# Kernel tuning notes

Hardware: AMD Instinct MI355X
Metric: run time of the kernel (lower is better)

## Reference

```python
import jax, jax.numpy as jnp
import numpy as np

L, H, C, V, BLK = 6, 16, 1024, 32000, 2048
B, T, TA = 2, 512, 512
DFF = 4 * C
STD = 0.02
PROJ_STD = 0.02 / np.sqrt(2 * L)  # c_proj init per module
SCALE = 1.0 / np.sqrt(C // H)


def setup_inputs() -> dict:
    key = jax.random.key(0)
    ks = iter(jax.random.split(key, 64))
    nrm = lambda shape, std=STD: jax.random.normal(next(ks), shape, jnp.float32) * std
    inp = {
        'idx': jax.random.randint(next(ks), (B, T), 0, V),
        'xa': jax.random.normal(next(ks), (B, TA, C), jnp.float32),
        'wte': nrm((V, C)),            # tied with lm_head
        'wpe': nrm((BLK, C)),
        'ln1_w': jnp.ones((L, C)), 'ln1_b': jnp.zeros((L, C)),
        'sa_wq': nrm((L, C, C)), 'sa_bq': jnp.zeros((L, C)),
        'sa_wk': nrm((L, C, C)), 'sa_bk': jnp.zeros((L, C)),
        'sa_wv': nrm((L, C, C)), 'sa_bv': jnp.zeros((L, C)),
        'sa_wo': nrm((L, C, C), PROJ_STD), 'sa_bo': jnp.zeros((L, C)),
        'ca_wq': nrm((L, C, C)), 'ca_bq': jnp.zeros((L, C)),
        'ca_wk': nrm((L, C, C)), 'ca_bk': jnp.zeros((L, C)),
        'ca_wv': nrm((L, C, C)), 'ca_bv': jnp.zeros((L, C)),
        'ca_wo': nrm((L, C, C), PROJ_STD), 'ca_bo': jnp.zeros((L, C)),
        'ln2_w': jnp.ones((L, C)), 'ln2_b': jnp.zeros((L, C)),
        'fc_w': nrm((L, C, DFF)), 'fc_b': jnp.zeros((L, DFF)),
        'pr_w': nrm((L, DFF, C), PROJ_STD), 'pr_b': jnp.zeros((L, C)),
        'lnf_w': jnp.ones((C,)), 'lnf_b': jnp.zeros((C,)),
    }
    return inp


def _ln(h, w, b):
    m = h.mean(-1, keepdims=True)
    v = jnp.mean((h - m) ** 2, -1, keepdims=True)
    return (h - m) * jax.lax.rsqrt(v + 1e-5) * w + b


def _gelu(h):  # new_gelu (tanh approximation)
    return 0.5 * h * (1.0 + jnp.tanh(np.sqrt(2.0 / np.pi) * (h + 0.044715 * h ** 3)))


def _attn(hq, hkv, wq, bq, wk, bk, wv, bv, wo, bo):
    # NB: the original applies a tril causal mask even for cross-attention.
    Bq, Tq, _ = hq.shape
    Tk = hkv.shape[1]
    D = C // H
    q = (hq @ wq + bq).reshape(Bq, Tq, H, D)
    k = (hkv @ wk + bk).reshape(Bq, Tk, H, D)
    v = (hkv @ wv + bv).reshape(Bq, Tk, H, D)
    att = jnp.einsum('bqhd,bkhd->bhqk', q, k) * SCALE
    mask = jnp.tril(jnp.ones((Tq, Tk), bool))
    att = jnp.where(mask, att, -jnp.inf)
    att = jax.nn.softmax(att, axis=-1)
    y = jnp.einsum('bhqk,bkhd->bqhd', att, v).reshape(Bq, Tq, C)
    return y @ wo + bo


def _forward(idx, xa, wte, wpe, ln1_w, ln1_b, sa_wq, sa_bq, sa_wk, sa_bk, sa_wv, sa_bv, sa_wo, sa_bo,
             ca_wq, ca_bq, ca_wk, ca_bk, ca_wv, ca_bv, ca_wo, ca_bo,
             ln2_w, ln2_b, fc_w, fc_b, pr_w, pr_b, lnf_w, lnf_b):
    t = idx.shape[1]
    x = wte[idx] + wpe[:t][None]  # [B,T,C]

    def block(h, p):
        (l1w, l1b, sqw, sqb, skw, skb, svw, svb, sow, sob,
         cqw, cqb, ckw, ckb, cvw, cvb, cow, cob,
         l2w, l2b, fw, fb, pw, pb) = p
        n = _ln(h, l1w, l1b)
        h = h + _attn(n, n, sqw, sqb, skw, skb, svw, svb, sow, sob)
        n = _ln(h, l1w, l1b)  # ln_1 reused for cross-attn, as in source
        h = h + _attn(n, xa, cqw, cqb, ckw, ckb, cvw, cvb, cow, cob)
        n = _ln(h, l2w, l2b)
        h = h + (_gelu(n @ fw + fb) @ pw + pb)
        return h, None

    xs = (ln1_w, ln1_b, sa_wq, sa_bq, sa_wk, sa_bk, sa_wv, sa_bv, sa_wo, sa_bo,
          ca_wq, ca_bq, ca_wk, ca_bk, ca_wv, ca_bv, ca_wo, ca_bo,
          ln2_w, ln2_b, fc_w, fc_b, pr_w, pr_b)
    x, _ = jax.lax.scan(block, x, xs)
    x = _ln(x, lnf_w, lnf_b)
    return x @ wte.T  # tied lm_head, [B,T,V]


def reference(idx, xa, wte, wpe, ln1_w, ln1_b, sa_wq, sa_bq, sa_wk, sa_bk, sa_wv, sa_bv, sa_wo, sa_bo,
              ca_wq, ca_bq, ca_wk, ca_bk, ca_wv, ca_bv, ca_wo, ca_bo,
              ln2_w, ln2_b, fc_w, fc_b, pr_w, pr_b, lnf_w, lnf_b):
    return _forward(idx, xa, wte, wpe, ln1_w, ln1_b, sa_wq, sa_bq, sa_wk, sa_bk, sa_wv, sa_bv, sa_wo, sa_bo,
                    ca_wq, ca_bq, ca_wk, ca_bk, ca_wv, ca_bv, ca_wo, ca_bo,
                    ln2_w, ln2_b, fc_w, fc_b, pr_w, pr_b, lnf_w, lnf_b)
```

## Files before the change

### kernel.cpp

```cpp
#include <hip/hip_runtime.h>
#include <math.h>

#define CC   1024
#define HH   16
#define DH   64
#define TT   512
#define NTOK 1024
#define DFF_ 4096
#define VV   32000
#define QKSCALE 0.125f

typedef unsigned short u16;
typedef __attribute__((ext_vector_type(8))) short short8;
typedef __attribute__((ext_vector_type(4))) float f32x4;

__device__ __forceinline__ u16 f2bf(float f) {
  union { float f; unsigned u; } v; v.f = f;
  unsigned r = v.u + 0x7FFFu + ((v.u >> 16) & 1u);
  return (u16)(r >> 16);
}
__device__ __forceinline__ float gelu_f(float h) {
  return 0.5f * h * (1.0f + tanhf(0.7978845608028654f * (h + 0.044715f * h * h * h)));
}

template <int N> __device__ __forceinline__ void waitcnt_vm() {
  if constexpr (N == 0) asm volatile("s_waitcnt vmcnt(0)" ::: "memory");
  else if constexpr (N == 1) asm volatile("s_waitcnt vmcnt(1)" ::: "memory");
  else if constexpr (N == 2) asm volatile("s_waitcnt vmcnt(2)" ::: "memory");
  else if constexpr (N == 3) asm volatile("s_waitcnt vmcnt(3)" ::: "memory");
  else if constexpr (N == 4) asm volatile("s_waitcnt vmcnt(4)" ::: "memory");
  else if constexpr (N == 5) asm volatile("s_waitcnt vmcnt(5)" ::: "memory");
  else if constexpr (N == 6) asm volatile("s_waitcnt vmcnt(6)" ::: "memory");
  else if constexpr (N == 7) asm volatile("s_waitcnt vmcnt(7)" ::: "memory");
  else if constexpr (N == 8) asm volatile("s_waitcnt vmcnt(8)" ::: "memory");
  else static_assert(N <= 8, "unsupported vmcnt");
}

#define GLD16(gp, lp) __builtin_amdgcn_global_load_lds( \
    (const __attribute__((address_space(1))) void*)(gp), \
    (__attribute__((address_space(3))) void*)(lp), 16, 0, 0)

#define MFMA(a, b, c) __builtin_amdgcn_mfma_f32_16x16x32_bf16(a, b, c, 0, 0, 0)

__global__ __launch_bounds__(256) void embed_kernel(
    const int* __restrict__ idx, const float* __restrict__ wte,
    const float* __restrict__ wpe, float* __restrict__ x) {
  int row = blockIdx.x;
  int t = row & (TT - 1);
  int id = idx[row];
  const float4* a = (const float4*)(wte + (size_t)id * CC);
  const float4* p = (const float4*)(wpe + (size_t)t * CC);
  float4* o = (float4*)(x + (size_t)row * CC);
  int c = threadIdx.x;
  float4 va = a[c], vp = p[c];
  float4 ov;
  ov.x = va.x + vp.x; ov.y = va.y + vp.y; ov.z = va.z + vp.z; ov.w = va.w + vp.w;
  o[c] = ov;
}

__global__ __launch_bounds__(256) void ln_kernel(
    const float* __restrict__ x, const float* __restrict__ w,
    const float* __restrict__ b, u16* __restrict__ out) {
  int row = blockIdx.x, tid = threadIdx.x;
  float4 v = ((const float4*)(x + (size_t)row * CC))[tid];
  float s  = v.x + v.y + v.z + v.w;
  float sq = fmaf(v.x, v.x, fmaf(v.y, v.y, fmaf(v.z, v.z, v.w * v.w)));
  for (int o = 32; o > 0; o >>= 1) { s += __shfl_down(s, o); sq += __shfl_down(sq, o); }
  __shared__ float rs[4], rq[4];
  int wid = tid >> 6, lane = tid & 63;
  if (lane == 0) { rs[wid] = s; rq[wid] = sq; }
  __syncthreads();
  s  = rs[0] + rs[1] + rs[2] + rs[3];
  sq = rq[0] + rq[1] + rq[2] + rq[3];
  float mean = s * (1.0f / CC);
  float var  = sq * (1.0f / CC) - mean * mean;
  float rstd = 1.0f / sqrtf(var + 1e-5f);
  float4 wv = ((const float4*)w)[tid];
  float4 bv = ((const float4*)b)[tid];
  ushort4 o;
  o.x = f2bf((v.x - mean) * rstd * wv.x + bv.x);
  o.y = f2bf((v.y - mean) * rstd * wv.y + bv.y);
  o.z = f2bf((v.z - mean) * rstd * wv.z + bv.z);
  o.w = f2bf((v.w - mean) * rstd * wv.w + bv.w);
  ((ushort4*)(out + (size_t)row * CC))[tid] = o;
}

__global__ __launch_bounds__(256) void wtransL_kernel(
    const float* __restrict__ w0, const float* __restrict__ w1,
    const float* __restrict__ w2, const float* __restrict__ w3,
    const float* __restrict__ w4, const float* __restrict__ w5,
    const float* __restrict__ w6, const float* __restrict__ w7,
    const float* __restrict__ fc, const float* __restrict__ pr,
    u16* __restrict__ wt, size_t dls, int lbase) {
  const size_t M1 = 1048576;
  int z = blockIdx.z;
  int l = lbase + (z >> 4), slot = z & 15;
  size_t wofs = (size_t)l * M1;
  size_t mofs = (size_t)l * 4 * M1;
  const float* src;
  size_t doff = (size_t)(l - lbase) * dls;
  int sstr, dstr;
  if (slot < 8) {
    const float* base = slot == 0 ? w0 : slot == 1 ? w1 : slot == 2 ? w2
                      : slot == 3 ? w3 : slot == 4 ? w4 : slot == 5 ? w5
                      : slot == 6 ? w6 : w7;
    src = base + wofs; sstr = 1024; doff += (size_t)slot * M1; dstr = 1024;
  } else if (slot < 12) {
    int s = slot - 8;
    src = fc + mofs + (size_t)s * 1024; sstr = 4096;
    doff += 8 * M1 + (size_t)s * M1; dstr = 1024;
  } else {
    int s = slot - 12;
    src = pr + mofs + (size_t)s * M1; sstr = 1024;
    doff += 12 * M1 + (size_t)s * 1024; dstr = 4096;
  }
  __shared__ float t[64][65];
  int bx = blockIdx.x * 64, by = blockIdx.y * 64;
  int tid = threadIdx.x;
  int r16 = tid >> 4;
  int c4  = (tid & 15) * 4;
#pragma unroll
  for (int i = 0; i < 4; ++i) {
    int row = r16 + i * 16;
    float4 v = *(const float4*)&src[(size_t)(by + row) * sstr + bx + c4];
    t[row][c4] = v.x; t[row][c4 + 1] = v.y; t[row][c4 + 2] = v.z; t[row][c4 + 3] = v.w;
  }
  __syncthreads();
#pragma unroll
  for (int i = 0; i < 4; ++i) {
    int orow = r16 + i * 16;
    ushort4 o;
    o.x = f2bf(t[c4 + 0][orow]);
    o.y = f2bf(t[c4 + 1][orow]);
    o.z = f2bf(t[c4 + 2][orow]);
    o.w = f2bf(t[c4 + 3][orow]);
    *(ushort4*)&wt[doff + (size_t)(bx + orow) * dstr + by + c4] = o;
  }
}

__global__ __launch_bounds__(256) void convbf_kernel(
    const float* __restrict__ in, u16* __restrict__ out, int n4) {
  int i = blockIdx.x * 256 + threadIdx.x;
  if (i < n4) {
    float4 v = ((const float4*)in)[i];
    ushort4 o; o.x = f2bf(v.x); o.y = f2bf(v.y); o.z = f2bf(v.z); o.w = f2bf(v.w);
    ((ushort4*)out)[i] = o;
  }
}

template <int EPI, int MODE, int BM, int BN, int BK, int SK>
__global__ __launch_bounds__(256) void gemm_bf16_kernel(
    const u16* __restrict__ A, const u16* __restrict__ A2,
    const u16* __restrict__ B, const u16* __restrict__ B2,
    const float* __restrict__ bias, const float* __restrict__ bias2,
    const float* __restrict__ bias3, float* __restrict__ Cm,
    int K, int ldc, int whichbase) {
  constexpr int WM = BM / 2, WN = BN / 2, MF = WM / 16, NF = WN / 16;
  constexpr int KS = BK / 32;
  constexpr int NB = BK / 8;
  constexpr int PA = BM * BK / 2048;
  constexpr int PB = BN * BK / 2048;
  constexpr int RPP = 2048 / BK;
  constexpr int NBUF = (MODE == 2) ? 2 : (MODE == 4 ? 1 : 3);
  __shared__ u16 As[NBUF][BM * BK];
  __shared__ u16 Bs[NBUF][BN * BK];
  int tid = threadIdx.x;
  int lane = tid & 63, wave = tid >> 6;
  int wr = wave >> 1, wc = wave & 1;
  int row0, col0;
  bool isq = true;
  const u16* Ause = A;
  const u16* Buse = B;
  if (MODE == 2 || MODE == 4) {
    int id = blockIdx.x;
    int wg = (id & 7) * 250 + (id >> 3);
    row0 = (wg & 7) * BM;
    col0 = (wg >> 3) * BN;
  } else if (MODE == 3) {
    int bx = blockIdx.x;
    isq = bx < (1024 / BN);
    Ause = isq ? A : A2;
    Buse = isq ? B : B2;
    col0 = (isq ? bx : bx - 1024 / BN) * BN;
    row0 = blockIdx.y * BM;
  } else {
    row0 = blockIdx.y * BM;
    col0 = blockIdx.x * BN;
  }
  const int split = (SK > 1) ? blockIdx.z : 0;
  const int Kloc = K / SK;
  const int kbase = split * Kloc;
  f32x4 acc[MF][NF];
#pragma unroll
  for (int m = 0; m < MF; ++m)
#pragma unroll
    for (int n = 0; n < NF; ++n) acc[m][n] = (f32x4){0.f, 0.f, 0.f, 0.f};

  int srow = tid / NB;
  int sblk = (BK == 64) ? ((tid & 7) ^ ((tid >> 3) & 7))
                        : ((tid & 3) ^ ((tid >> 3) & 3));
  const u16* Ab = Ause + (size_t)row0 * K + kbase;
  int arow = wr * WM + (lane & 15);
  int brow = wc * WN + (lane & 15);
  int g8 = lane >> 4;
  const int NT = Kloc / BK;

  auto compute = [&](const u16* Ac, const u16* Bc) {
#pragma unroll
    for (int ks = 0; ks < KS; ++ks) {
      short8 af[MF], bg[NF];
#pragma unroll
      for (int m = 0; m < MF; ++m) {
        int row = arow + m * 16;
        int off = (BK == 64) ? row * 64 + (((ks * 4 + g8) ^ (row & 7)) << 3)
                             : row * 32 + ((g8 ^ ((row >> 1) & 3)) << 3);
        af[m] = *(const short8*)&Ac[off];
      }
#pragma unroll
      for (int n = 0; n < NF; ++n) {
        int row = brow + n * 16;
        int off = (BK == 64) ? row * 64 + (((ks * 4 + g8) ^ (row & 7)) << 3)
                             : row * 32 + ((g8 ^ ((row >> 1) & 3)) << 3);
        bg[n] = *(const short8*)&Bc[off];
      }
      __builtin_amdgcn_s_setprio(1);
#pragma unroll
      for (int m = 0; m < MF; ++m)
#pragma unroll
        for (int n = 0; n < NF; ++n)
          acc[m][n] = MFMA(af[m], bg[n], acc[m][n]);
      __builtin_amdgcn_s_setprio(0);
    }
  };

  if constexpr (MODE == 2) {
    const float* Bf = (const float*)B;
    int bsr = tid >> 2;
    int bkb = tid & 3;
    float4 rb0, rb1, rb2, rb3;
    auto loadB = [&](int k0) {
      const float* p0 = Bf + (size_t)(col0 + bsr) * 1024 + k0 + bkb * 8;
      const float* p1 = Bf + (size_t)(col0 + 64 + bsr) * 1024 + k0 + bkb * 8;
      rb0 = *(const float4*)p0; rb1 = *(const float4*)(p0 + 4);
      rb2 = *(const float4*)p1; rb3 = *(const float4*)(p1 + 4);
    };
    auto writeB = [&](int bufi) {
      u16 t0[8] = {f2bf(rb0.x), f2bf(rb0.y), f2bf(rb0.z), f2bf(rb0.w),
                   f2bf(rb1.x), f2bf(rb1.y), f2bf(rb1.z), f2bf(rb1.w)};
      u16 t1[8] = {f2bf(rb2.x), f2bf(rb2.y), f2bf(rb2.z), f2bf(rb2.w),
                   f2bf(rb3.x), f2bf(rb3.y), f2bf(rb3.z), f2bf(rb3.w)};
      int r1 = 64 + bsr;
      *(short8*)&Bs[bufi][bsr * 32 + ((bkb ^ ((bsr >> 1) & 3)) << 3)] = *(short8*)t0;
      *(short8*)&Bs[bufi][r1 * 32 + ((bkb ^ ((r1 >> 1) & 3)) << 3)] = *(short8*)t1;
    };
    auto stageA = [&](int bufi, int k0) {
#pragma unroll
      for (int p = 0; p < PA; ++p)
        GLD16(Ab + (size_t)(p * RPP + srow) * K + k0 + sblk * 8,
              &As[bufi][p * 2048 + wave * 512]);
    };
    loadB(0);
    stageA(0, 0);
    writeB(0);
    __syncthreads();
    for (int t = 0; t < NT; ++t) {
      int cur = t & 1;
      if (t + 1 < NT) { loadB((t + 1) * BK); stageA(cur ^ 1, (t + 1) * BK); }
      compute(As[cur], Bs[cur]);
      if (t + 1 < NT) writeB(cur ^ 1);
      __syncthreads();
    }
  } else if constexpr (MODE == 4) {
    const u16* Bb = Buse + (size_t)col0 * K + kbase;
    for (int t = 0; t < NT; ++t) {
      int k0 = t * BK;
#pragma unroll
      for (int p = 0; p < PA; ++p)
        GLD16(Ab + (size_t)(p * RPP + srow) * K + k0 + sblk * 8,
              &As[0][p * 2048 + wave * 512]);
#pragma unroll
      for (int p = 0; p < PB; ++p)
        GLD16(Bb + (size_t)(p * RPP + srow) * K + k0 + sblk * 8,
              &Bs[0][p * 2048 + wave * 512]);
      __syncthreads();
      compute(As[0], Bs[0]);
      __syncthreads();
    }
  } else {
    const u16* Bb = Buse + (size_t)col0 * K + kbase;
    auto stage = [&](int bufi, int k0) {
#pragma unroll
      for (int p = 0; p < PA; ++p)
        GLD16(Ab + (size_t)(p * RPP + srow) * K + k0 + sblk * 8,
              &As[bufi][p * 2048 + wave * 512]);
#pragma unroll
      for (int p = 0; p < PB; ++p)
        GLD16(Bb + (size_t)(p * RPP + srow) * K + k0 + sblk * 8,
              &Bs[bufi][p * 2048 + wave * 512]);
    };
    stage(0, 0);
    if (NT > 1) stage(1, BK);
    for (int t = 0; t < NT; ++t) {
      if (t + 1 < NT) waitcnt_vm<PA + PB>();
      else            waitcnt_vm<0>();
      __builtin_amdgcn_s_barrier();
      __builtin_amdgcn_sched_barrier(0);
      if (t + 2 < NT) stage((t + 2) % 3, (t + 2) * BK);
      int cur = t % 3;
      compute(As[cur], Bs[cur]);
    }
  }

  int r0 = row0 + wr * WM + g8 * 4;
  int c0 = col0 + wc * WN + (lane & 15);

  if (EPI == 4) {
    u16* qb = (u16*)Cm;
#pragma unroll
    for (int m = 0; m < MF; ++m)
#pragma unroll
      for (int n = 0; n < NF; ++n) {
        int j = c0 + n * 16;
        int which = (MODE == 3 ? (isq ? 0 : 1) : whichbase) + (j >> 10);
        const float* bp = which == 0 ? bias : (which == 1 ? bias2 : bias3);
        float bj = bp ? bp[j & 1023] : 0.0f;
        int h = (j & 1023) >> 6, d = j & 63;
        int trow0 = r0 + m * 16;
        int b = trow0 >> 9, t0 = trow0 & 511;
        int bh = b * 16 + h;
        u16 vals[4];
#pragma unroll
        for (int r = 0; r < 4; ++r) vals[r] = f2bf(acc[m][n][r] + bj);
        if (which < 2) {
          u16* dst = qb + (size_t)which * 1048576 + (size_t)bh * 32768 + (size_t)t0 * 64 + d;
#pragma unroll
          for (int r = 0; r < 4; ++r) dst[(size_t)r * 64] = vals[r];
        } else {
          u16* dst = qb + 2 * 1048576 + (size_t)bh * 32768 + (size_t)d * 512 + t0;
          *(ushort4*)dst = *(ushort4*)vals;
        }
      }
    return;
  }

  float bj[NF];
#pragma unroll
  for (int n = 0; n < NF; ++n)
    bj[n] = bias ? bias[c0 + n * 16] : 0.0f;
  u16* Cb = (u16*)Cm;
#pragma unroll
  for (int m = 0; m < MF; ++m)
#pragma unroll
    for (int n = 0; n < NF; ++n)
#pragma unroll
      for (int r = 0; r < 4; ++r) {
        size_t off = (size_t)(r0 + m * 16 + r) * ldc + c0 + n * 16;
        float v = acc[m][n][r] + ((SK == 1 || split == 0) ? bj[n] : 0.0f);
        if (EPI == 0) Cm[off] = v;
        else if (EPI == 1) {
          if constexpr (SK > 1) atomicAdd(&Cm[off], v);
          else Cm[off] += v;
        }
        else if (EPI == 2) Cb[off] = f2bf(gelu_f(v));
      }
}

__global__ __launch_bounds__(256) void attn_kernel(
    const u16* __restrict__ qh, const u16* __restrict__ kh,
    const u16* __restrict__ vt, u16* __restrict__ y) {
  __shared__ u16 P[32 * 512];
  __shared__ float smax[4][32], ssum[4][32];
  int tid = threadIdx.x, lane = tid & 63, w = tid >> 6;
  int bx = blockIdx.x, bh = blockIdx.y;
  int q0 = bx * 32;
  int b = bh >> 4, h = bh & 15;
  const u16* qb = qh + (size_t)bh * 32768;
  const u16* kb = kh + (size_t)bh * 32768;
  const u16* vb = vt + (size_t)bh * 32768;
  int g = lane >> 4, c = lane & 15;

  short8 a[2][2];
#pragma unroll
  for (int rt = 0; rt < 2; ++rt)
#pragma unroll
    for (int ks = 0; ks < 2; ++ks)
      a[rt][ks] = *(const short8*)(qb + (size_t)(q0 + rt * 16 + c) * 64 + ks * 32 + g * 8);

  int lim = q0 + 31;
  int nct = (lim - w * 128) / 16 + 1;
  if (nct > 8) nct = 8;
  if (nct < 0) nct = 0;
  f32x4 s[2][8];
#pragma unroll
  for (int rt = 0; rt < 2; ++rt)
#pragma unroll
    for (int ct = 0; ct < 8; ++ct) s[rt][ct] = (f32x4){0.f, 0.f, 0.f, 0.f};
  for (int ct = 0; ct < nct; ++ct) {
    int n0 = w * 128 + ct * 16;
#pragma unroll
    for (int ks = 0; ks < 2; ++ks) {
      short8 bf = *(const short8*)(kb + (size_t)(n0 + c) * 64 + ks * 32 + g * 8);
      s[0][ct] = MFMA(a[0][ks], bf, s[0][ct]);
      s[1][ct] = MFMA(a[1][ks], bf, s[1][ct]);
    }
  }

  float mx[2][4];
#pragma unroll
  for (int rt = 0; rt < 2; ++rt)
#pragma unroll
    for (int r = 0; r < 4; ++r) mx[rt][r] = -1e30f;
  for (int ct = 0; ct < nct; ++ct) {
    int col = w * 128 + ct * 16 + c;
#pragma unroll
    for (int rt = 0; rt < 2; ++rt)
#pragma unroll
      for (int r = 0; r < 4; ++r) {
        int trow = q0 + rt * 16 + g * 4 + r;
        float v = s[rt][ct][r] * QKSCALE;
        if (col > trow) v = -1e30f;
        s[rt][ct][r] = v;
        mx[rt][r] = fmaxf(mx[rt][r], v);
      }
  }
#pragma unroll
  for (int off = 1; off < 16; off <<= 1)
#pragma unroll
    for (int rt = 0; rt < 2; ++rt)
#pragma unroll
      for (int r = 0; r < 4; ++r) mx[rt][r] = fmaxf(mx[rt][r], __shfl_xor(mx[rt][r], off));
  if (c == 0)
#pragma unroll
    for (int rt = 0; rt < 2; ++rt)
#pragma unroll
      for (int r = 0; r < 4; ++r) smax[w][rt * 16 + g * 4 + r] = mx[rt][r];
  __syncthreads();

  float m_[2][4], sum[2][4];
#pragma unroll
  for (int rt = 0; rt < 2; ++rt)
#pragma unroll
    for (int r = 0; r < 4; ++r) {
      int row = rt * 16 + g * 4 + r;
      m_[rt][r] = fmaxf(fmaxf(smax[0][row], smax[1][row]), fmaxf(smax[2][row], smax[3][row]));
      sum[rt][r] = 0.f;
    }
  for (int ct = 0; ct < nct; ++ct) {
    int col = w * 128 + ct * 16 + c;
    int blk = col >> 3, cl = col & 7;
#pragma unroll
    for (int rt = 0; rt < 2; ++rt)
#pragma unroll
      for (int r = 0; r < 4; ++r) {
        float p = __expf(s[rt][ct][r] - m_[rt][r]);
        sum[rt][r] += p;
        int row = rt * 16 + g * 4 + r;
        int hsh = (row ^ (row >> 2)) & 7;
        P[row * 512 + ((blk ^ hsh) << 3) + cl] = f2bf(p);
      }
  }
#pragma unroll
  for (int off = 1; off < 16; off <<= 1)
#pragma unroll
    for (int rt = 0; rt < 2; ++rt)
#pragma unroll
      for (int r = 0; r < 4; ++r) sum[rt][r] += __shfl_xor(sum[rt][r], off);
  if (c == 0)
#pragma unroll
    for (int rt = 0; rt < 2; ++rt)
#pragma unroll
      for (int r = 0; r < 4; ++r) ssum[w][rt * 16 + g * 4 + r] = sum[rt][r];
  __syncthreads();

  float li[2][4];
#pragma unroll
  for (int rt = 0; rt < 2; ++rt)
#pragma unroll
    for (int r = 0; r < 4; ++r) {
      int row = rt * 16 + g * 4 + r;
      li[rt][r] = 1.0f / (ssum[0][row] + ssum[1][row] + ssum[2][row] + ssum[3][row]);
    }

  int rt2 = w >> 1, nh = w & 1;
  f32x4 o[2];
  o[0] = (f32x4){0.f, 0.f, 0.f, 0.f};
  o[1] = (f32x4){0.f, 0.f, 0.f, 0.f};
  int nks = bx + 1;
  int prow = rt2 * 16 + c;
  int phsh = (prow ^ (prow >> 2)) & 7;
  for (int ks = 0; ks < nks; ++ks) {
    short8 pa = *(const short8*)&P[prow * 512 + (((ks * 4 + g) ^ phsh) << 3)];
#pragma unroll
    for (int nt = 0; nt < 2; ++nt) {
      int d = nh * 32 + nt * 16 + c;
      short8 vf = *(const short8*)(vb + (size_t)d * 512 + ks * 32 + g * 8);
      o[nt] = MFMA(pa, vf, o[nt]);
    }
  }
#pragma unroll
  for (int nt = 0; nt < 2; ++nt)
#pragma unroll
    for (int r = 0; r < 4; ++r) {
      int trow = q0 + rt2 * 16 + g * 4 + r;
      float val = o[nt][r] * li[rt2][r];
      y[(size_t)(b * 512 + trow) * 1024 + h * 64 + nh * 32 + nt * 16 + c] = f2bf(val);
    }
}

extern "C" void kernel_launch(void* const* d_in, const int* in_sizes, int n_in,
                              void* d_out, int out_size, void* d_ws, size_t ws_size,
                              hipStream_t stream) {
  const int*   idx   = (const int*)d_in[0];
  const float* xa    = (const float*)d_in[1];
  const float* wte   = (const float*)d_in[2];
  const float* wpe   = (const float*)d_in[3];
  const float* ln1_w = (const float*)d_in[4];
  const float* ln1_b = (const float*)d_in[5];
  const float* sa_wq = (const float*)d_in[6];
  const float* sa_bq = (const float*)d_in[7];
  const float* sa_wk = (const float*)d_in[8];
  const float* sa_bk = (const float*)d_in[9];
  const float* sa_wv = (const float*)d_in[10];
  const float* sa_bv = (const float*)d_in[11];
  const float* sa_wo = (const float*)d_in[12];
  const float* sa_bo = (const float*)d_in[13];
  const float* ca_wq = (const float*)d_in[14];
  const float* ca_bq = (const float*)d_in[15];
  const float* ca_wk = (const float*)d_in[16];
  const float* ca_bk = (const float*)d_in[17];
  const float* ca_wv = (const float*)d_in[18];
  const float* ca_bv = (const float*)d_in[19];
  const float* ca_wo = (const float*)d_in[20];
  const float* ca_bo = (const float*)d_in[21];
  const float* ln2_w = (const float*)d_in[22];
  const float* ln2_b = (const float*)d_in[23];
  const float* fc_w  = (const float*)d_in[24];
  const float* fc_b  = (const float*)d_in[25];
  const float* pr_w  = (const float*)d_in[26];
  const float* pr_b  = (const float*)d_in[27];
  const float* lnf_w = (const float*)d_in[28];
  const float* lnf_b = (const float*)d_in[29];

  const size_t M1 = 1048576;
  float* ws     = (float*)d_ws;
  float* x      = ws;
  u16* qkvh  = (u16*)(x + M1);
  u16* nbf   = qkvh + 3 * M1;
  u16* ybf   = nbf + M1;
  u16* hmbf  = ybf + M1;
  u16* xabf  = hmbf + 4 * M1;

  const bool fullW = ws_size >= 292028416ull;
  const bool full  = fullW || ws_size >= 226492416ull;
  u16* wtebf = xabf + M1;
  u16* wT    = fullW ? wtebf + (size_t)VV * CC : xabf + M1;
  const size_t wls = full ? 16 * M1 : 0;

  const size_t oQKV = 0, oWO = 3 * M1, oCQ = 4 * M1, oCKV = 5 * M1,
               oCWO = 7 * M1, oFC = 8 * M1, oPR = 12 * M1;

  embed_kernel<<<NTOK, 256, 0, stream>>>(idx, wte, wpe, x);
  convbf_kernel<<<(NTOK * CC / 4 + 255) / 256, 256, 0, stream>>>(xa, xabf, NTOK * CC / 4);
  if (fullW)
    convbf_kernel<<<(VV * CC / 4 + 255) / 256, 256, 0, stream>>>(wte, wtebf, VV * CC / 4);
  if (full)
    wtransL_kernel<<<dim3(16, 16, 96), 256, 0, stream>>>(
        sa_wq, sa_wk, sa_wv, sa_wo, ca_wq, ca_wk, ca_wv, ca_wo,
        fc_w, pr_w, wT, wls, 0);

  for (int l = 0; l < 6; ++l) {
    size_t bofs = (size_t)l * CC;
    u16* wTl = wT + (size_t)l * wls;

    if (!full)
      wtransL_kernel<<<dim3(16, 16, 16), 256, 0, stream>>>(
          sa_wq, sa_wk, sa_wv, sa_wo, ca_wq, ca_wk, ca_wv, ca_wo,
          fc_w, pr_w, wT, 0, l);

    ln_kernel<<<NTOK, 256, 0, stream>>>(x, ln1_w + bofs, ln1_b + bofs, nbf);
    gemm_bf16_kernel<4, 0, 64, 128, 64, 1><<<dim3(24, 16), 256, 0, stream>>>(
        nbf, nullptr, wTl + oQKV, nullptr, sa_bq + bofs, sa_bk + bofs,
        sa_bv + bofs, (float*)qkvh, CC, 0, 0);
    attn_kernel<<<dim3(16, 32), 256, 0, stream>>>(qkvh, qkvh + M1, qkvh + 2 * M1, ybf);
    gemm_bf16_kernel<1, 0, 32, 64, 64, 2><<<dim3(16, 32, 2), 256, 0, stream>>>(
        ybf, nullptr, wTl + oWO, nullptr, sa_bo + bofs, nullptr, nullptr,
        x, CC, CC, 0);

    ln_kernel<<<NTOK, 256, 0, stream>>>(x, ln1_w + bofs, ln1_b + bofs, nbf);
    gemm_bf16_kernel<4, 3, 64, 64, 64, 1><<<dim3(48, 16), 256, 0, stream>>>(
        nbf, xabf, wTl + oCQ, wTl + oCKV, ca_bq + bofs, ca_bk + bofs,
        ca_bv + bofs, (float*)qkvh, CC, 0, 0);
    attn_kernel<<<dim3(16, 32), 256, 0, stream>>>(qkvh, qkvh + M1, qkvh + 2 * M1, ybf);
    gemm_bf16_kernel<1, 0, 32, 64, 64, 2><<<dim3(16, 32, 2), 256, 0, stream>>>(
        ybf, nullptr, wTl + oCWO, nullptr, ca_bo + bofs, nullptr, nullptr,
        x, CC, CC, 0);

    ln_kernel<<<NTOK, 256, 0, stream>>>(x, ln2_w + bofs, ln2_b + bofs, nbf);
    gemm_bf16_kernel<2, 0, 64, 128, 64, 1><<<dim3(32, 16), 256, 0, stream>>>(
        nbf, nullptr, wTl + oFC, nullptr, fc_b + (size_t)l * DFF_, nullptr,
        nullptr, (float*)hmbf, CC, DFF_, 0);
    gemm_bf16_kernel<1, 0, 32, 64, 64, 4><<<dim3(16, 32, 4), 256, 0, stream>>>(
        hmbf, nullptr, wTl + oPR, nullptr, pr_b + bofs, nullptr, nullptr,
        x, DFF_, CC, 0);
  }

  ln_kernel<<<NTOK, 256, 0, stream>>>(x, lnf_w, lnf_b, nbf);
  if (fullW)
    gemm_bf16_kernel<0, 4, 128, 128, 64, 1><<<dim3(2000), 256, 0, stream>>>(
        nbf, nullptr, wtebf, nullptr, nullptr, nullptr, nullptr,
        (float*)d_out, CC, VV, 0);
  else
    gemm_bf16_kernel<0, 2, 128, 128, 32, 1><<<dim3(2000), 256, 0, stream>>>(
        nbf, nullptr, (const u16*)wte, nullptr, nullptr, nullptr, nullptr,
        (float*)d_out, CC, VV, 0);
}
```

Before: 1.509 ms.

## Pair causal attention query tiles per block and fuse wte conversion into weight prep

The attention kernel now has each block handle two query tiles, bx and 15-bx, in sequence. This balances the causal-mask work across blocks and halves the grid. Separately, the wte fp32-to-bf16 conversion is folded into the weight-transpose kernel as extra z-slices, which removes one launch and lets both run concurrently. The trade-offs are fewer blocks for attention, and therefore less parallelism on a large GPU, plus an added __syncthreads between the two halves.

```diff
diff --git a/kernel.cpp b/kernel.cpp
--- a/kernel.cpp
+++ b/kernel.cpp
@@ -91,9 +91,22 @@
     const float* __restrict__ w4, const float* __restrict__ w5,
     const float* __restrict__ w6, const float* __restrict__ w7,
     const float* __restrict__ fc, const float* __restrict__ pr,
-    u16* __restrict__ wt, size_t dls, int lbase) {
+    u16* __restrict__ wt, size_t dls, int lbase, int nl,
+    const float* __restrict__ wte, u16* __restrict__ wtebf) {
   const size_t M1 = 1048576;
   int z = blockIdx.z;
+  if (z >= nl * 16) {
+    int slot = z - nl * 16;
+    int blin = blockIdx.y * 16 + blockIdx.x;
+    const int n4 = VV * CC / 4;
+    int gi = (slot * 256 + blin) * 256 + threadIdx.x;
+    for (int i = gi; i < n4; i += 32 * 256 * 256) {
+      float4 v = ((const float4*)wte)[i];
+      ushort4 o; o.x = f2bf(v.x); o.y = f2bf(v.y); o.z = f2bf(v.z); o.w = f2bf(v.w);
+      ((ushort4*)wtebf)[i] = o;
+    }
+    return;
+  }
   int l = lbase + (z >> 4), slot = z & 15;
   size_t wofs = (size_t)l * M1;
   size_t mofs = (size_t)l * 4 * M1;
@@ -371,140 +384,145 @@
   __shared__ u16 P[32 * 512];
   __shared__ float smax[4][32], ssum[4][32];
   int tid = threadIdx.x, lane = tid & 63, w = tid >> 6;
-  int bx = blockIdx.x, bh = blockIdx.y;
-  int q0 = bx * 32;
+  int bh = blockIdx.y;
   int b = bh >> 4, h = bh & 15;
   const u16* qb = qh + (size_t)bh * 32768;
   const u16* kb = kh + (size_t)bh * 32768;
   const u16* vb = vt + (size_t)bh * 32768;
   int g = lane >> 4, c = lane & 15;
 
-  short8 a[2][2];
-#pragma unroll
-  for (int rt = 0; rt < 2; ++rt)
-#pragma unroll
-    for (int ks = 0; ks < 2; ++ks)
-      a[rt][ks] = *(const short8*)(qb + (size_t)(q0 + rt * 16 + c) * 64 + ks * 32 + g * 8);
-
-  int lim = q0 + 31;
-  int nct = (lim - w * 128) / 16 + 1;
-  if (nct > 8) nct = 8;
-  if (nct < 0) nct = 0;
-  f32x4 s[2][8];
-#pragma unroll
-  for (int rt = 0; rt < 2; ++rt)
-#pragma unroll
-    for (int ct = 0; ct < 8; ++ct) s[rt][ct] = (f32x4){0.f, 0.f, 0.f, 0.f};
-  for (int ct = 0; ct < nct; ++ct) {
-    int n0 = w * 128 + ct * 16;
-#pragma unroll
-    for (int ks = 0; ks < 2; ++ks) {
-      short8 bf = *(const short8*)(kb + (size_t)(n0 + c) * 64 + ks * 32 + g * 8);
-      s[0][ct] = MFMA(a[0][ks], bf, s[0][ct]);
-      s[1][ct] = MFMA(a[1][ks], bf, s[1][ct]);
-    }
-  }
-
-  float mx[2][4];
-#pragma unroll
-  for (int rt = 0; rt < 2; ++rt)
-#pragma unroll
-    for (int r = 0; r < 4; ++r) mx[rt][r] = -1e30f;
-  for (int ct = 0; ct < nct; ++ct) {
-    int col = w * 128 + ct * 16 + c;
+  for (int half = 0; half < 2; ++half) {
+    int bx = half == 0 ? (int)blockIdx.x : 15 - (int)blockIdx.x;
+    if (half) __syncthreads();
+    int q0 = bx * 32;
+
+    short8 a[2][2];
 #pragma unroll
     for (int rt = 0; rt < 2; ++rt)
 #pragma unroll
+      for (int ks = 0; ks < 2; ++ks)
+        a[rt][ks] = *(const short8*)(qb + (size_t)(q0 + rt * 16 + c) * 64 + ks * 32 + g * 8);
+
+    int lim = q0 + 31;
+    int nct = (lim - w * 128) / 16 + 1;
+    if (nct > 8) nct = 8;
+    if (nct < 0) nct = 0;
+    f32x4 s[2][8];
+#pragma unroll
+    for (int rt = 0; rt < 2; ++rt)
+#pragma unroll
+      for (int ct = 0; ct < 8; ++ct) s[rt][ct] = (f32x4){0.f, 0.f, 0.f, 0.f};
+    for (int ct = 0; ct < nct; ++ct) {
+      int n0 = w * 128 + ct * 16;
+#pragma unroll
+      for (int ks = 0; ks < 2; ++ks) {
+        short8 bf = *(const short8*)(kb + (size_t)(n0 + c) * 64 + ks * 32 + g * 8);
+        s[0][ct] = MFMA(a[0][ks], bf, s[0][ct]);
+        s[1][ct] = MFMA(a[1][ks], bf, s[1][ct]);
+      }
+    }
+
+    float mx[2][4];
+#pragma unroll
+    for (int rt = 0; rt < 2; ++rt)
+#pragma unroll
+      for (int r = 0; r < 4; ++r) mx[rt][r] = -1e30f;
+    for (int ct = 0; ct < nct; ++ct) {
+      int col = w * 128 + ct * 16 + c;
+#pragma unroll
+      for (int rt = 0; rt < 2; ++rt)
+#pragma unroll
+        for (int r = 0; r < 4; ++r) {
+          int trow = q0 + rt * 16 + g * 4 + r;
+          float v = s[rt][ct][r] * QKSCALE;
+          if (col > trow) v = -1e30f;
+          s[rt][ct][r] = v;
+          mx[rt][r] = fmaxf(mx[rt][r], v);
+        }
+    }
+#pragma unroll
+    for (int off = 1; off < 16; off <<= 1)
+#pragma unroll
+      for (int rt = 0; rt < 2; ++rt)
+#pragma unroll
+        for (int r = 0; r < 4; ++r) mx[rt][r] = fmaxf(mx[rt][r], __shfl_xor(mx[rt][r], off));
+    if (c == 0)
+#pragma unroll
+      for (int rt = 0; rt < 2; ++rt)
+#pragma unroll
+        for (int r = 0; r < 4; ++r) smax[w][rt * 16 + g * 4 + r] = mx[rt][r];
+    __syncthreads();
+
+    float m_[2][4], sum[2][4];
+#pragma unroll
+    for (int rt = 0; rt < 2; ++rt)
+#pragma unroll
       for (int r = 0; r < 4; ++r) {
-        int trow = q0 + rt * 16 + g * 4 + r;
-        float v = s[rt][ct][r] * QKSCALE;
-        if (col > trow) v = -1e30f;
-        s[rt][ct][r] = v;
-        mx[rt][r] = fmaxf(mx[rt][r], v);
-      }
-  }
-#pragma unroll
-  for (int off = 1; off < 16; off <<= 1)
+        int row = rt * 16 + g * 4 + r;
+        m_[rt][r] = fmaxf(fmaxf(smax[0][row], smax[1][row]), fmaxf(smax[2][row], smax[3][row]));
+        sum[rt][r] = 0.f;
+      }
+    for (int ct = 0; ct < nct; ++ct) {
+      int col = w * 128 + ct * 16 + c;
+      int blk = col >> 3, cl = col & 7;
+#pragma unroll
+      for (int rt = 0; rt < 2; ++rt)
+#pragma unroll
+        for (int r = 0; r < 4; ++r) {
+          float p = __expf(s[rt][ct][r] - m_[rt][r]);
+          sum[rt][r] += p;
+          int row = rt * 16 + g * 4 + r;
+          int hsh = (row ^ (row >> 2)) & 7;
+          P[row * 512 + ((blk ^ hsh) << 3) + cl] = f2bf(p);
+        }
+    }
+#pragma unroll
+    for (int off = 1; off < 16; off <<= 1)
+#pragma unroll
+      for (int rt = 0; rt < 2; ++rt)
+#pragma unroll
+        for (int r = 0; r < 4; ++r) sum[rt][r] += __shfl_xor(sum[rt][r], off);
+    if (c == 0)
+#pragma unroll
+      for (int rt = 0; rt < 2; ++rt)
+#pragma unroll
+        for (int r = 0; r < 4; ++r) ssum[w][rt * 16 + g * 4 + r] = sum[rt][r];
+    __syncthreads();
+
+    float li[2][4];
 #pragma unroll
     for (int rt = 0; rt < 2; ++rt)
 #pragma unroll
-      for (int r = 0; r < 4; ++r) mx[rt][r] = fmaxf(mx[rt][r], __shfl_xor(mx[rt][r], off));
-  if (c == 0)
-#pragma unroll
-    for (int rt = 0; rt < 2; ++rt)
-#pragma unroll
-      for (int r = 0; r < 4; ++r) smax[w][rt * 16 + g * 4 + r] = mx[rt][r];
-  __syncthreads();
-
-  float m_[2][4], sum[2][4];
-#pragma unroll
-  for (int rt = 0; rt < 2; ++rt)
-#pragma unroll
-    for (int r = 0; r < 4; ++r) {
-      int row = rt * 16 + g * 4 + r;
-      m_[rt][r] = fmaxf(fmaxf(smax[0][row], smax[1][row]), fmaxf(smax[2][row], smax[3][row]));
-      sum[rt][r] = 0.f;
-    }
-  for (int ct = 0; ct < nct; ++ct) {
-    int col = w * 128 + ct * 16 + c;
-    int blk = col >> 3, cl = col & 7;
-#pragma unroll
-    for (int rt = 0; rt < 2; ++rt)
-#pragma unroll
       for (int r = 0; r < 4; ++r) {
-        float p = __expf(s[rt][ct][r] - m_[rt][r]);
-        sum[rt][r] += p;
         int row = rt * 16 + g * 4 + r;
-        int hsh = (row ^ (row >> 2)) & 7;
-        P[row * 512 + ((blk ^ hsh) << 3) + cl] = f2bf(p);
-      }
-  }
-#pragma unroll
-  for (int off = 1; off < 16; off <<= 1)
-#pragma unroll
-    for (int rt = 0; rt < 2; ++rt)
-#pragma unroll
-      for (int r = 0; r < 4; ++r) sum[rt][r] += __shfl_xor(sum[rt][r], off);
-  if (c == 0)
-#pragma unroll
-    for (int rt = 0; rt < 2; ++rt)
-#pragma unroll
-      for (int r = 0; r < 4; ++r) ssum[w][rt * 16 + g * 4 + r] = sum[rt][r];
-  __syncthreads();
-
-  float li[2][4];
-#pragma unroll
-  for (int rt = 0; rt < 2; ++rt)
-#pragma unroll
-    for (int r = 0; r < 4; ++r) {
-      int row = rt * 16 + g * 4 + r;
-      li[rt][r] = 1.0f / (ssum[0][row] + ssum[1][row] + ssum[2][row] + ssum[3][row]);
-    }
-
-  int rt2 = w >> 1, nh = w & 1;
-  f32x4 o[2];
-  o[0] = (f32x4){0.f, 0.f, 0.f, 0.f};
-  o[1] = (f32x4){0.f, 0.f, 0.f, 0.f};
-  int nks = bx + 1;
-  int prow = rt2 * 16 + c;
-  int phsh = (prow ^ (prow >> 2)) & 7;
-  for (int ks = 0; ks < nks; ++ks) {
-    short8 pa = *(const short8*)&P[prow * 512 + (((ks * 4 + g) ^ phsh) << 3)];
-#pragma unroll
-    for (int nt = 0; nt < 2; ++nt) {
-      int d = nh * 32 + nt * 16 + c;
-      short8 vf = *(const short8*)(vb + (size_t)d * 512 + ks * 32 + g * 8);
-      o[nt] = MFMA(pa, vf, o[nt]);
-    }
-  }
-#pragma unroll
-  for (int nt = 0; nt < 2; ++nt)
-#pragma unroll
-    for (int r = 0; r < 4; ++r) {
-      int trow = q0 + rt2 * 16 + g * 4 + r;
-      float val = o[nt][r] * li[rt2][r];
-      y[(size_t)(b * 512 + trow) * 1024 + h * 64 + nh * 32 + nt * 16 + c] = f2bf(val);
-    }
+        li[rt][r] = 1.0f / (ssum[0][row] + ssum[1][row] + ssum[2][row] + ssum[3][row]);
+      }
+
+    int rt2 = w >> 1, nh = w & 1;
+    f32x4 o[2];
+    o[0] = (f32x4){0.f, 0.f, 0.f, 0.f};
+    o[1] = (f32x4){0.f, 0.f, 0.f, 0.f};
+    int nks = bx + 1;
+    int prow = rt2 * 16 + c;
+    int phsh = (prow ^ (prow >> 2)) & 7;
+    for (int ks = 0; ks < nks; ++ks) {
+      short8 pa = *(const short8*)&P[prow * 512 + (((ks * 4 + g) ^ phsh) << 3)];
+#pragma unroll
+      for (int nt = 0; nt < 2; ++nt) {
+        int d = nh * 32 + nt * 16 + c;
+        short8 vf = *(const short8*)(vb + (size_t)d * 512 + ks * 32 + g * 8);
+        o[nt] = MFMA(pa, vf, o[nt]);
+      }
+    }
+#pragma unroll
+    for (int nt = 0; nt < 2; ++nt)
+#pragma unroll
+      for (int r = 0; r < 4; ++r) {
+        int trow = q0 + rt2 * 16 + g * 4 + r;
+        float val = o[nt][r] * li[rt2][r];
+        y[(size_t)(b * 512 + trow) * 1024 + h * 64 + nh * 32 + nt * 16 + c] = f2bf(val);
+      }
+  }
 }
 
 extern "C" void kernel_launch(void* const* d_in, const int* in_sizes, int n_in,
@@ -561,12 +579,12 @@
 
   embed_kernel<<<NTOK, 256, 0, stream>>>(idx, wte, wpe, x);
   convbf_kernel<<<(NTOK * CC / 4 + 255) / 256, 256, 0, stream>>>(xa, xabf, NTOK * CC / 4);
-  if (fullW)
-    convbf_kernel<<<(VV * CC / 4 + 255) / 256, 256, 0, stream>>>(wte, wtebf, VV * CC / 4);
-  if (full)
-    wtransL_kernel<<<dim3(16, 16, 96), 256, 0, stream>>>(
+  if (full) {
+    int nz = fullW ? 96 + 32 : 96;
+    wtransL_kernel<<<dim3(16, 16, nz), 256, 0, stream>>>(
         sa_wq, sa_wk, sa_wv, sa_wo, ca_wq, ca_wk, ca_wv, ca_wo,
-        fc_w, pr_w, wT, wls, 0);
+        fc_w, pr_w, wT, wls, 0, 6, wte, wtebf);
+  }
 
   for (int l = 0; l < 6; ++l) {
     size_t bofs = (size_t)l * CC;
@@ -575,13 +593,13 @@
     if (!full)
       wtransL_kernel<<<dim3(16, 16, 16), 256, 0, stream>>>(
           sa_wq, sa_wk, sa_wv, sa_wo, ca_wq, ca_wk, ca_wv, ca_wo,
-          fc_w, pr_w, wT, 0, l);
+          fc_w, pr_w, wT, 0, l, 6, nullptr, nullptr);
 
     ln_kernel<<<NTOK, 256, 0, stream>>>(x, ln1_w + bofs, ln1_b + bofs, nbf);
     gemm_bf16_kernel<4, 0, 64, 128, 64, 1><<<dim3(24, 16), 256, 0, stream>>>(
         nbf, nullptr, wTl + oQKV, nullptr, sa_bq + bofs, sa_bk + bofs,
         sa_bv + bofs, (float*)qkvh, CC, 0, 0);
-    attn_kernel<<<dim3(16, 32), 256, 0, stream>>>(qkvh, qkvh + M1, qkvh + 2 * M1, ybf);
+    attn_kernel<<<dim3(8, 32), 256, 0, stream>>>(qkvh, qkvh + M1, qkvh + 2 * M1, ybf);
     gemm_bf16_kernel<1, 0, 32, 64, 64, 2><<<dim3(16, 32, 2), 256, 0, stream>>>(
         ybf, nullptr, wTl + oWO, nullptr, sa_bo + bofs, nullptr, nullptr,
         x, CC, CC, 0);
@@ -590,7 +608,7 @@
     gemm_bf16_kernel<4, 3, 64, 64, 64, 1><<<dim3(48, 16), 256, 0, stream>>>(
         nbf, xabf, wTl + oCQ, wTl + oCKV, ca_bq + bofs, ca_bk + bofs,
         ca_bv + bofs, (float*)qkvh, CC, 0, 0);
-    attn_kernel<<<dim3(16, 32), 256, 0, stream>>>(qkvh, qkvh + M1, qkvh + 2 * M1, ybf);
+    attn_kernel<<<dim3(8, 32), 256, 0, stream>>>(qkvh, qkvh + M1, qkvh + 2 * M1, ybf);
     gemm_bf16_kernel<1, 0, 32, 64, 64, 2><<<dim3(16, 32, 2), 256, 0, stream>>>(
         ybf, nullptr, wTl + oCWO, nullptr, ca_bo + bofs, nullptr, nullptr,
         x, CC, CC, 0);
```

Measured after the change: 1.487 ms. No clear change (-1.5%).
